# Performance work log

Measured on AMD Instinct MI355X. Metric: run time of the kernel, lower is better.

Reference implementation:

```python
import jax, jax.numpy as jnp
import numpy as np

B, T, I, H = 64, 512, 1024, 1024

def setup_inputs() -> dict:
    key = jax.random.key(0)
    k1, k2, k3, k4, k5 = jax.random.split(key, 5)
    s_x = 1.0 / np.sqrt(I)
    s_h = 1.0 / np.sqrt(H)
    return {
        "x": jax.random.normal(k1, (B, T, I), dtype=jnp.float32),
        "Wx": jax.random.uniform(k2, (I, H), minval=-s_x, maxval=s_x, dtype=jnp.float32),
        "bx": jax.random.uniform(k3, (H,), minval=-s_x, maxval=s_x, dtype=jnp.float32),
        "Wh": jax.random.uniform(k4, (H, H), minval=-s_h, maxval=s_h, dtype=jnp.float32),
        "bh": jax.random.uniform(k5, (H,), minval=-s_h, maxval=s_h, dtype=jnp.float32),
    }

def reference(x, Wx, bx, Wh, bh):
    # Precompute input projections for all timesteps in one big GEMM: [B,T,H]
    xproj = jnp.einsum("bti,ih->bth", x, Wx) + bx + bh
    h0 = jnp.zeros((x.shape[0], Wh.shape[0]), dtype=x.dtype)

    def step(h, xp_t):
        h_new = jnp.tanh(xp_t + h @ Wh)
        return h_new, h_new

    # scan over time: xproj transposed to [T,B,H]
    h_last, outs = jax.lax.scan(step, h0, jnp.swapaxes(xproj, 0, 1))
    return jnp.swapaxes(outs, 0, 1), h_last
```

## Files before the change

### kernel.cpp

```cpp
#include <hip/hip_runtime.h>


#define Bdim 64
#define Tdim 512
#define Idim 1024
#define Hdim 1024
#define Mdim (Bdim * Tdim)

typedef __attribute__((ext_vector_type(8))) short bf16x8;
typedef __attribute__((ext_vector_type(4))) float f32x4;
typedef __attribute__((ext_vector_type(4))) unsigned int u32x4;

__device__ __forceinline__ float tanh_fast(float x) {
  float e = __expf(2.0f * x);
  return 1.0f - 2.0f / (e + 1.0f);
}
__device__ __forceinline__ unsigned int f2bf(float f) {
  unsigned int u = __float_as_uint(f);
  return (u + 0x7FFFu + ((u >> 16) & 1u)) >> 16;
}
__device__ __forceinline__ unsigned int pack2(float lo, float hi) {
  return f2bf(lo) | (f2bf(hi) << 16);
}

__global__ __launch_bounds__(256) void cvt_transpose(
    const float* __restrict__ src, unsigned short* __restrict__ dst) {
  __shared__ float t[32][33];
  const int bx = blockIdx.x * 32;
  const int by = blockIdx.y * 32;
  const int ty = threadIdx.x >> 3;
  const int tx = threadIdx.x & 7;
  float4 v = *(const float4*)&src[(size_t)(by + ty) * 1024 + bx + tx * 4];
  t[ty][tx * 4 + 0] = v.x; t[ty][tx * 4 + 1] = v.y;
  t[ty][tx * 4 + 2] = v.z; t[ty][tx * 4 + 3] = v.w;
  __syncthreads();
  ushort4 o;
  o.x = (unsigned short)f2bf(t[tx * 4 + 0][ty]);
  o.y = (unsigned short)f2bf(t[tx * 4 + 1][ty]);
  o.z = (unsigned short)f2bf(t[tx * 4 + 2][ty]);
  o.w = (unsigned short)f2bf(t[tx * 4 + 3][ty]);
  *(ushort4*)&dst[(size_t)(bx + ty) * 1024 + by + tx * 4] = o;
}

__global__ __launch_bounds__(256) void xg_mfma(
    const float* __restrict__ X,
    const unsigned short* __restrict__ WxT,
    const float* __restrict__ bx, const float* __restrict__ bh,
    float* __restrict__ C) {
  __shared__ char sAB[16384] __attribute__((aligned(16)));
  char* sA = sAB;
  char* sB = sAB + 8192;
  const int tid = threadIdx.x;
  const int m0 = blockIdx.y * 128;
  const int n0 = blockIdx.x * 128;
  const int w = tid >> 6, l = tid & 63;
  const int wm = (w >> 1) * 64, wn = (w & 1) * 64;
  const int r2 = tid >> 1, kh = tid & 1;

  f32x4 acc[4][4];
#pragma unroll
  for (int i = 0; i < 4; ++i)
#pragma unroll
    for (int j = 0; j < 4; ++j) acc[i][j] = (f32x4){0.f, 0.f, 0.f, 0.f};

  for (int k0 = 0; k0 < Idim; k0 += 32) {
    const float* xa = &X[(size_t)(m0 + r2) * Idim + k0 + kh * 16];
    float4 a0 = *(const float4*)(xa + 0), a1 = *(const float4*)(xa + 4);
    float4 a2 = *(const float4*)(xa + 8), a3 = *(const float4*)(xa + 12);
    const char* wb = (const char*)&WxT[(size_t)(n0 + r2) * Idim + k0 + kh * 16];
    u32x4 b0 = *(const u32x4*)wb;
    u32x4 b1 = *(const u32x4*)(wb + 16);
    __syncthreads();
    u32x4 pa0 = {pack2(a0.x, a0.y), pack2(a0.z, a0.w),
                 pack2(a1.x, a1.y), pack2(a1.z, a1.w)};
    u32x4 pa1 = {pack2(a2.x, a2.y), pack2(a2.z, a2.w),
                 pack2(a3.x, a3.y), pack2(a3.z, a3.w)};
    const int sw = (r2 & 7) << 4;
    const int rb = r2 * 64 + kh * 32;
    *(u32x4*)(sA + ((rb + 0) ^ sw)) = pa0;
    *(u32x4*)(sA + ((rb + 16) ^ sw)) = pa1;
    *(u32x4*)(sB + ((rb + 0) ^ sw)) = b0;
    *(u32x4*)(sB + ((rb + 16) ^ sw)) = b1;
    __syncthreads();
    bf16x8 af[4], bf[4];
#pragma unroll
    for (int i = 0; i < 4; ++i) {
      int ra = wm + i * 16 + (l & 15);
      af[i] = *(const bf16x8*)(sA + ((ra * 64 + (l >> 4) * 16) ^ ((ra & 7) << 4)));
      int rn = wn + i * 16 + (l & 15);
      bf[i] = *(const bf16x8*)(sB + ((rn * 64 + (l >> 4) * 16) ^ ((rn & 7) << 4)));
    }
#pragma unroll
    for (int i = 0; i < 4; ++i)
#pragma unroll
      for (int j = 0; j < 4; ++j)
        acc[i][j] = __builtin_amdgcn_mfma_f32_16x16x32_bf16(af[i], bf[j],
                                                            acc[i][j], 0, 0, 0);
  }
  float bias[4];
#pragma unroll
  for (int j = 0; j < 4; ++j) {
    int cc = n0 + wn + j * 16 + (l & 15);
    bias[j] = bx[cc] + bh[cc];
  }
#pragma unroll
  for (int i = 0; i < 4; ++i) {
    int rbase = m0 + wm + i * 16 + (l >> 4) * 4;
#pragma unroll
    for (int j = 0; j < 4; ++j) {
      int cc = n0 + wn + j * 16 + (l & 15);
#pragma unroll
      for (int r = 0; r < 4; ++r)
        C[(size_t)(rbase + r) * Hdim + cc] = acc[i][j][r] + bias[j];
    }
  }
}

__global__ void clear_flags(unsigned int* flags) {
  __hip_atomic_store(&flags[threadIdx.x], 0u, __ATOMIC_RELAXED,
                     __HIP_MEMORY_SCOPE_AGENT);
}

__global__ __launch_bounds__(512, 2) void rnn_scan(
    const unsigned short* __restrict__ WhT,
    float* __restrict__ out,
    float* __restrict__ hlast,
    unsigned int* hbuf,
    unsigned int* flags) {
  const int bid = blockIdx.x;
  const int c = bid & 7;
  const int m = bid >> 3;
  const int tid = threadIdx.x;
  const int w = tid >> 6;
  const int l = tid & 63;
  const int n0 = m * 128;

  __shared__ char smem[16384 + 33792] __attribute__((aligned(16)));
  char* const smh = smem;
  char* const smp = smem + 16384;

  bf16x8 bfrag[32];
  {
    const int kb = (w << 7) + ((l >> 4) << 3);
    const int col = n0 + (l & 15);
#pragma unroll
    for (int nt = 0; nt < 8; ++nt)
#pragma unroll
      for (int kt = 0; kt < 4; ++kt)
        bfrag[nt * 4 + kt] =
            *(const bf16x8*)&WhT[(size_t)(col + nt * 16) * 1024 + kb + kt * 32];
  }
#pragma unroll
  for (int i = 0; i < 32; ++i) asm volatile("" : "+v"(bfrag[i]));

  const int c0 = l * 2;
  const int b_abs = c * 8 + w;
  const int nt0 = c0 >> 4;
  const int lane0 = ((w >> 2) << 4) | (c0 & 15);
  const int regb = (w & 3) * 4;
  const size_t orow = (size_t)b_abs * ((size_t)Tdim * Hdim) + n0 + c0;
  unsigned int* const myflag = &flags[c * 32 + m];
  const unsigned int* const pollf = &flags[c * 32 + (l & 7)];

  float2 xp = *(const float2*)&out[orow];

  for (int t = 0; t < Tdim; ++t) {
    float sum0 = 0.f, sum1 = 0.f;
    if (t > 0) {
      const int arow = l & 7;
      const int ab = arow * 2048 + (w << 8) + ((l >> 4) << 4);
      const int sw2 = arow << 4;
      bf16x8 af0 = *(const bf16x8*)(smh + ((ab + 0) ^ sw2));
      bf16x8 af1 = *(const bf16x8*)(smh + ((ab + 64) ^ sw2));
      bf16x8 af2 = *(const bf16x8*)(smh + ((ab + 128) ^ sw2));
      bf16x8 af3 = *(const bf16x8*)(smh + ((ab + 192) ^ sw2));
#pragma unroll
      for (int nt = 0; nt < 8; ++nt) {
        f32x4 a = {0.f, 0.f, 0.f, 0.f};
        a = __builtin_amdgcn_mfma_f32_16x16x32_bf16(af0, bfrag[nt * 4 + 0], a, 0, 0, 0);
        a = __builtin_amdgcn_mfma_f32_16x16x32_bf16(af1, bfrag[nt * 4 + 1], a, 0, 0, 0);
        a = __builtin_amdgcn_mfma_f32_16x16x32_bf16(af2, bfrag[nt * 4 + 2], a, 0, 0, 0);
        a = __builtin_amdgcn_mfma_f32_16x16x32_bf16(af3, bfrag[nt * 4 + 3], a, 0, 0, 0);
        if (l < 32)
          *(f32x4*)(smp + (((w * 8 + nt) * 33 + l) << 4)) = a;
      }
      asm volatile("s_waitcnt lgkmcnt(0)" ::: "memory");
      __builtin_amdgcn_s_barrier();
      asm volatile("" ::: "memory");
#pragma unroll
      for (int w8 = 0; w8 < 8; ++w8) {
        const char* p = smp + (((w8 * 8 + nt0) * 33 + lane0) << 4) + regb;
        sum0 += *(const float*)p;
        sum1 += *(const float*)(p + 16);
      }
    }
    float h0 = tanh_fast(xp.x + sum0);
    float h1 = tanh_fast(xp.y + sum1);
    if (t == Tdim - 1) {
      *(float2*)&out[orow + (size_t)t * Hdim] = make_float2(h0, h1);
      *(float2*)&hlast[(size_t)b_abs * Hdim + n0 + c0] = make_float2(h0, h1);
      break;
    }
    const int par = (t + 1) & 1;
    const unsigned int tp1 = (unsigned int)(t + 1);
    {
      unsigned int* pubp = hbuf + (size_t)par * 32768 + (size_t)b_abs * 512 +
                           m * 64 + l;
      unsigned int pv = pack2(h0, h1);
      asm volatile("global_store_dword %0, %1, off sc0 sc1"
                   :: "v"(pubp), "v"(pv) : "memory");
    }
    if (w != 7) {
      *(float2*)&out[orow + (size_t)t * Hdim] = make_float2(h0, h1);
      xp = *(const float2*)&out[orow + (size_t)(t + 1) * Hdim];
      asm volatile("s_waitcnt vmcnt(2)" ::: "memory");
    } else {
      asm volatile("s_waitcnt vmcnt(0)" ::: "memory");
    }
    __builtin_amdgcn_s_barrier();
    asm volatile("" ::: "memory");
    if (tid == 0)
      __hip_atomic_store(myflag, tp1, __ATOMIC_RELAXED,
                         __HIP_MEMORY_SCOPE_AGENT);
    if (w == 7) {
      for (;;) {
        unsigned int v;
        asm volatile(
            "global_load_dword %0, %1, off sc0 sc1\n\ts_waitcnt vmcnt(0)"
            : "=v"(v) : "v"(pollf) : "memory");
        if (__ballot(v >= tp1) == ~0ull) break;
        __builtin_amdgcn_s_sleep(1);
      }
    }
    __builtin_amdgcn_s_barrier();
    asm volatile("" ::: "memory");
    {
      const char* srcp = (const char*)hbuf + (size_t)par * 131072 +
                         (size_t)b_abs * 2048 + l * 32;
      u32x4 d0, d1;
      asm volatile(
          "global_load_dwordx4 %0, %2, off sc0 sc1\n\t"
          "global_load_dwordx4 %1, %2, off offset:16 sc0 sc1\n\t"
          "s_waitcnt vmcnt(0)"
          : "=&v"(d0), "=&v"(d1) : "v"(srcp) : "memory");
      __builtin_amdgcn_sched_barrier(0);
      const int base = w * 2048 + l * 32;
      const int swz = w << 4;
      *(u32x4*)(smh + (base ^ swz)) = d0;
      *(u32x4*)(smh + ((base + 16) ^ swz)) = d1;
    }
    if (w == 7) {
      *(float2*)&out[orow + (size_t)t * Hdim] = make_float2(h0, h1);
      xp = *(const float2*)&out[orow + (size_t)(t + 1) * Hdim];
    }
    asm volatile("s_waitcnt lgkmcnt(0)" ::: "memory");
    __builtin_amdgcn_s_barrier();
    asm volatile("" ::: "memory");
  }
}

extern "C" void kernel_launch(void* const* d_in, const int* in_sizes, int n_in,
                              void* d_out, int out_size, void* d_ws,
                              size_t ws_size, hipStream_t stream) {
  const float* x  = (const float*)d_in[0];
  const float* Wx = (const float*)d_in[1];
  const float* bx = (const float*)d_in[2];
  const float* Wh = (const float*)d_in[3];
  const float* bh = (const float*)d_in[4];
  float* out = (float*)d_out;
  float* hlast = out + (size_t)Bdim * Tdim * Hdim;
  unsigned int* flags = (unsigned int*)d_ws;
  unsigned int* hbuf = (unsigned int*)((char*)d_ws + 4096);
  unsigned short* WxT = (unsigned short*)((char*)d_ws + 4096 + 262144);
  unsigned short* WhT = (unsigned short*)((char*)d_ws + 4096 + 262144 + 2097152);

  clear_flags<<<1, dim3(256), 0, stream>>>(flags);
  dim3 gt(32, 32);
  cvt_transpose<<<gt, dim3(256), 0, stream>>>(Wx, WxT);
  cvt_transpose<<<gt, dim3(256), 0, stream>>>(Wh, WhT);
  xg_mfma<<<dim3(Hdim / 128, Mdim / 128), dim3(256), 0, stream>>>(x, WxT, bx,
                                                                  bh, out);
  rnn_scan<<<dim3(64), dim3(512), 0, stream>>>(WhT, out, hlast, hbuf, flags);
}
```

Measured before the change: 1.561 ms.

## Load recurrent A fragments directly from global, drop LDS staging and barrier

Each wave now loads its bf16 MFMA A-fragments of the previous hidden state straight from the global exchange buffer into registers. Previously each wave cooperatively copied an 8-row slab into swizzled shared memory, then read fragments back after an extra barrier. This removes the shared-memory staging, one barrier and the LDS pressure per timestep. In exchange it issues four scattered global loads per lane on the critical path instead of two contiguous ones, and the out store and xproj prefetch now sit after the poll rather than overlapping the flag wait.

```diff
diff --git a/kernel.cpp b/kernel.cpp
--- a/kernel.cpp
+++ b/kernel.cpp
@@ -135,9 +135,7 @@
   const int l = tid & 63;
   const int n0 = m * 128;
 
-  __shared__ char smem[16384 + 33792] __attribute__((aligned(16)));
-  char* const smh = smem;
-  char* const smp = smem + 16384;
+  __shared__ char smp[33792] __attribute__((aligned(16)));
 
   bf16x8 bfrag[32];
   {
@@ -161,19 +159,15 @@
   const size_t orow = (size_t)b_abs * ((size_t)Tdim * Hdim) + n0 + c0;
   unsigned int* const myflag = &flags[c * 32 + m];
   const unsigned int* const pollf = &flags[c * 32 + (l & 7)];
+  const char* const afbase = (const char*)hbuf +
+      (size_t)(c * 8 + (l & 7)) * 2048 + (size_t)((w << 8) + ((l >> 4) << 4));
 
   float2 xp = *(const float2*)&out[orow];
+  bf16x8 af0 = {}, af1 = {}, af2 = {}, af3 = {};
 
   for (int t = 0; t < Tdim; ++t) {
     float sum0 = 0.f, sum1 = 0.f;
     if (t > 0) {
-      const int arow = l & 7;
-      const int ab = arow * 2048 + (w << 8) + ((l >> 4) << 4);
-      const int sw2 = arow << 4;
-      bf16x8 af0 = *(const bf16x8*)(smh + ((ab + 0) ^ sw2));
-      bf16x8 af1 = *(const bf16x8*)(smh + ((ab + 64) ^ sw2));
-      bf16x8 af2 = *(const bf16x8*)(smh + ((ab + 128) ^ sw2));
-      bf16x8 af3 = *(const bf16x8*)(smh + ((ab + 192) ^ sw2));
 #pragma unroll
       for (int nt = 0; nt < 8; ++nt) {
         f32x4 a = {0.f, 0.f, 0.f, 0.f};
@@ -207,15 +201,9 @@
       unsigned int* pubp = hbuf + (size_t)par * 32768 + (size_t)b_abs * 512 +
                            m * 64 + l;
       unsigned int pv = pack2(h0, h1);
-      asm volatile("global_store_dword %0, %1, off sc0 sc1"
-                   :: "v"(pubp), "v"(pv) : "memory");
-    }
-    if (w != 7) {
-      *(float2*)&out[orow + (size_t)t * Hdim] = make_float2(h0, h1);
-      xp = *(const float2*)&out[orow + (size_t)(t + 1) * Hdim];
-      asm volatile("s_waitcnt vmcnt(2)" ::: "memory");
-    } else {
-      asm volatile("s_waitcnt vmcnt(0)" ::: "memory");
+      asm volatile(
+          "global_store_dword %0, %1, off sc0 sc1\n\ts_waitcnt vmcnt(0)"
+          :: "v"(pubp), "v"(pv) : "memory");
     }
     __builtin_amdgcn_s_barrier();
     asm volatile("" ::: "memory");
@@ -235,27 +223,19 @@
     __builtin_amdgcn_s_barrier();
     asm volatile("" ::: "memory");
     {
-      const char* srcp = (const char*)hbuf + (size_t)par * 131072 +
-                         (size_t)b_abs * 2048 + l * 32;
-      u32x4 d0, d1;
+      const char* srcp = afbase + (size_t)par * 131072;
       asm volatile(
-          "global_load_dwordx4 %0, %2, off sc0 sc1\n\t"
-          "global_load_dwordx4 %1, %2, off offset:16 sc0 sc1\n\t"
+          "global_load_dwordx4 %0, %4, off sc0 sc1\n\t"
+          "global_load_dwordx4 %1, %4, off offset:64 sc0 sc1\n\t"
+          "global_load_dwordx4 %2, %4, off offset:128 sc0 sc1\n\t"
+          "global_load_dwordx4 %3, %4, off offset:192 sc0 sc1\n\t"
           "s_waitcnt vmcnt(0)"
-          : "=&v"(d0), "=&v"(d1) : "v"(srcp) : "memory");
+          : "=&v"(af0), "=&v"(af1), "=&v"(af2), "=&v"(af3)
+          : "v"(srcp) : "memory");
       __builtin_amdgcn_sched_barrier(0);
-      const int base = w * 2048 + l * 32;
-      const int swz = w << 4;
-      *(u32x4*)(smh + (base ^ swz)) = d0;
-      *(u32x4*)(smh + ((base + 16) ^ swz)) = d1;
-    }
-    if (w == 7) {
-      *(float2*)&out[orow + (size_t)t * Hdim] = make_float2(h0, h1);
-      xp = *(const float2*)&out[orow + (size_t)(t + 1) * Hdim];
-    }
-    asm volatile("s_waitcnt lgkmcnt(0)" ::: "memory");
-    __builtin_amdgcn_s_barrier();
-    asm volatile("" ::: "memory");
+    }
+    *(float2*)&out[orow + (size_t)t * Hdim] = make_float2(h0, h1);
+    xp = *(const float2*)&out[orow + (size_t)(t + 1) * Hdim];
   }
 }
 
```

Result: slower. 1.867 ms (+19.6%).

## Fuse input-projection GEMM into recurrent scan kernel with per-time-chunk gating

Applied to the files above, without the earlier changes.

Merges the input-projection GEMM and the recurrent scan into one launch. 64 blocks run the scan while the remaining blocks compute GEMM tiles with 128x256 tiles. Each GEMM tile bumps a counter for its 128-timestep chunk, and the scan waits on that counter before entering each chunk. This is meant to hide most of the GEMM time behind the serial, latency-bound scan. The risks are that GEMM blocks compete with the scan blocks for CU time and memory bandwidth, and that the design depends on co-residency for forward progress. It also simplifies the per-step store and wait ordering and slightly lengthens the poll sleep.

```diff
diff --git a/kernel.cpp b/kernel.cpp
--- a/kernel.cpp
+++ b/kernel.cpp
@@ -42,100 +42,106 @@
   *(ushort4*)&dst[(size_t)(bx + ty) * 1024 + by + tx * 4] = o;
 }
 
-__global__ __launch_bounds__(256) void xg_mfma(
-    const float* __restrict__ X,
-    const unsigned short* __restrict__ WxT,
-    const float* __restrict__ bx, const float* __restrict__ bh,
-    float* __restrict__ C) {
-  __shared__ char sAB[16384] __attribute__((aligned(16)));
-  char* sA = sAB;
-  char* sB = sAB + 8192;
-  const int tid = threadIdx.x;
-  const int m0 = blockIdx.y * 128;
-  const int n0 = blockIdx.x * 128;
-  const int w = tid >> 6, l = tid & 63;
-  const int wm = (w >> 1) * 64, wn = (w & 1) * 64;
-  const int r2 = tid >> 1, kh = tid & 1;
-
-  f32x4 acc[4][4];
-#pragma unroll
-  for (int i = 0; i < 4; ++i)
-#pragma unroll
-    for (int j = 0; j < 4; ++j) acc[i][j] = (f32x4){0.f, 0.f, 0.f, 0.f};
-
-  for (int k0 = 0; k0 < Idim; k0 += 32) {
-    const float* xa = &X[(size_t)(m0 + r2) * Idim + k0 + kh * 16];
-    float4 a0 = *(const float4*)(xa + 0), a1 = *(const float4*)(xa + 4);
-    float4 a2 = *(const float4*)(xa + 8), a3 = *(const float4*)(xa + 12);
-    const char* wb = (const char*)&WxT[(size_t)(n0 + r2) * Idim + k0 + kh * 16];
-    u32x4 b0 = *(const u32x4*)wb;
-    u32x4 b1 = *(const u32x4*)(wb + 16);
-    __syncthreads();
-    u32x4 pa0 = {pack2(a0.x, a0.y), pack2(a0.z, a0.w),
-                 pack2(a1.x, a1.y), pack2(a1.z, a1.w)};
-    u32x4 pa1 = {pack2(a2.x, a2.y), pack2(a2.z, a2.w),
-                 pack2(a3.x, a3.y), pack2(a3.z, a3.w)};
-    const int sw = (r2 & 7) << 4;
-    const int rb = r2 * 64 + kh * 32;
-    *(u32x4*)(sA + ((rb + 0) ^ sw)) = pa0;
-    *(u32x4*)(sA + ((rb + 16) ^ sw)) = pa1;
-    *(u32x4*)(sB + ((rb + 0) ^ sw)) = b0;
-    *(u32x4*)(sB + ((rb + 16) ^ sw)) = b1;
-    __syncthreads();
-    bf16x8 af[4], bf[4];
-#pragma unroll
-    for (int i = 0; i < 4; ++i) {
-      int ra = wm + i * 16 + (l & 15);
-      af[i] = *(const bf16x8*)(sA + ((ra * 64 + (l >> 4) * 16) ^ ((ra & 7) << 4)));
-      int rn = wn + i * 16 + (l & 15);
-      bf[i] = *(const bf16x8*)(sB + ((rn * 64 + (l >> 4) * 16) ^ ((rn & 7) << 4)));
-    }
-#pragma unroll
-    for (int i = 0; i < 4; ++i)
-#pragma unroll
-      for (int j = 0; j < 4; ++j)
-        acc[i][j] = __builtin_amdgcn_mfma_f32_16x16x32_bf16(af[i], bf[j],
-                                                            acc[i][j], 0, 0, 0);
-  }
-  float bias[4];
-#pragma unroll
-  for (int j = 0; j < 4; ++j) {
-    int cc = n0 + wn + j * 16 + (l & 15);
-    bias[j] = bx[cc] + bh[cc];
-  }
-#pragma unroll
-  for (int i = 0; i < 4; ++i) {
-    int rbase = m0 + wm + i * 16 + (l >> 4) * 4;
-#pragma unroll
-    for (int j = 0; j < 4; ++j) {
-      int cc = n0 + wn + j * 16 + (l & 15);
-#pragma unroll
-      for (int r = 0; r < 4; ++r)
-        C[(size_t)(rbase + r) * Hdim + cc] = acc[i][j][r] + bias[j];
-    }
-  }
-}
-
 __global__ void clear_flags(unsigned int* flags) {
   __hip_atomic_store(&flags[threadIdx.x], 0u, __ATOMIC_RELAXED,
                      __HIP_MEMORY_SCOPE_AGENT);
 }
 
-__global__ __launch_bounds__(512, 2) void rnn_scan(
+__global__ __launch_bounds__(512, 2) void fused(
+    const float* __restrict__ X,
+    const unsigned short* __restrict__ WxT,
     const unsigned short* __restrict__ WhT,
+    const float* __restrict__ bx, const float* __restrict__ bh,
     float* __restrict__ out,
     float* __restrict__ hlast,
-    unsigned int* hbuf,
-    unsigned int* flags) {
+    unsigned int* hbuf, unsigned int* flags) {
+  __shared__ char smem[50176] __attribute__((aligned(16)));
+  unsigned int* counters = flags + 256;
   const int bid = blockIdx.x;
-  const int c = bid & 7;
-  const int m = bid >> 3;
   const int tid = threadIdx.x;
   const int w = tid >> 6;
   const int l = tid & 63;
+
+  if (bid >= 64) {
+    const int gid = bid - 64;
+    const int mt = gid >> 2;
+    const int np = gid & 3;
+    const int m0 = mt * 128, n0 = np * 256;
+    const int tc = mt & 3;
+    char* const sA = smem;
+    char* const sB = smem + 8192;
+    const int half = w >> 2, w2 = w & 3;
+    const int wm = (w2 >> 1) * 64, wn = half * 128 + (w2 & 1) * 64;
+    const int rA = tid >> 2, kA = tid & 3;
+    const int rB = tid >> 1, kB = tid & 1;
+
+    f32x4 acc[4][4];
+#pragma unroll
+    for (int i = 0; i < 4; ++i)
+#pragma unroll
+      for (int j = 0; j < 4; ++j) acc[i][j] = (f32x4){0.f, 0.f, 0.f, 0.f};
+
+    for (int k0 = 0; k0 < Idim; k0 += 32) {
+      const float* xa = &X[(size_t)(m0 + rA) * Idim + k0 + kA * 8];
+      float4 a0 = *(const float4*)xa, a1 = *(const float4*)(xa + 4);
+      const char* wb =
+          (const char*)&WxT[(size_t)(n0 + rB) * Idim + k0 + kB * 16];
+      u32x4 b0 = *(const u32x4*)wb, b1 = *(const u32x4*)(wb + 16);
+      __syncthreads();
+      u32x4 pa = {pack2(a0.x, a0.y), pack2(a0.z, a0.w),
+                  pack2(a1.x, a1.y), pack2(a1.z, a1.w)};
+      *(u32x4*)(sA + ((rA * 64 + kA * 16) ^ ((rA & 7) << 4))) = pa;
+      const int rbB = rB * 64 + kB * 32, swB = (rB & 7) << 4;
+      *(u32x4*)(sB + (rbB ^ swB)) = b0;
+      *(u32x4*)(sB + ((rbB + 16) ^ swB)) = b1;
+      __syncthreads();
+      bf16x8 af[4], bf[4];
+#pragma unroll
+      for (int i = 0; i < 4; ++i) {
+        int ra = wm + i * 16 + (l & 15);
+        af[i] = *(const bf16x8*)(sA + ((ra * 64 + (l >> 4) * 16) ^ ((ra & 7) << 4)));
+        int rn = wn + i * 16 + (l & 15);
+        bf[i] = *(const bf16x8*)(sB + ((rn * 64 + (l >> 4) * 16) ^ ((rn & 7) << 4)));
+      }
+#pragma unroll
+      for (int i = 0; i < 4; ++i)
+#pragma unroll
+        for (int j = 0; j < 4; ++j)
+          acc[i][j] = __builtin_amdgcn_mfma_f32_16x16x32_bf16(af[i], bf[j],
+                                                              acc[i][j], 0, 0, 0);
+    }
+    float bias[4];
+#pragma unroll
+    for (int j = 0; j < 4; ++j) {
+      int cc = n0 + wn + j * 16 + (l & 15);
+      bias[j] = bx[cc] + bh[cc];
+    }
+#pragma unroll
+    for (int i = 0; i < 4; ++i) {
+      int rbase = m0 + wm + i * 16 + (l >> 4) * 4;
+#pragma unroll
+      for (int j = 0; j < 4; ++j) {
+        int cc = n0 + wn + j * 16 + (l & 15);
+#pragma unroll
+        for (int r = 0; r < 4; ++r) {
+          float v = acc[i][j][r] + bias[j];
+          float* p = &out[(size_t)(rbase + r) * Hdim + cc];
+          asm volatile("global_store_dword %0, %1, off sc0 sc1"
+                       :: "v"(p), "v"(v) : "memory");
+        }
+      }
+    }
+    asm volatile("s_waitcnt vmcnt(0)" ::: "memory");
+    __syncthreads();
+    if (tid == 0)
+      __hip_atomic_fetch_add(&counters[tc], 1u, __ATOMIC_RELAXED,
+                             __HIP_MEMORY_SCOPE_AGENT);
+    return;
+  }
+
+  const int c = bid & 7;
+  const int m = bid >> 3;
   const int n0 = m * 128;
-
-  __shared__ char smem[16384 + 33792] __attribute__((aligned(16)));
   char* const smh = smem;
   char* const smp = smem + 16384;
 
@@ -150,8 +156,6 @@
         bfrag[nt * 4 + kt] =
             *(const bf16x8*)&WhT[(size_t)(col + nt * 16) * 1024 + kb + kt * 32];
   }
-#pragma unroll
-  for (int i = 0; i < 32; ++i) asm volatile("" : "+v"(bfrag[i]));
 
   const int c0 = l * 2;
   const int b_abs = c * 8 + w;
@@ -162,6 +166,22 @@
   unsigned int* const myflag = &flags[c * 32 + m];
   const unsigned int* const pollf = &flags[c * 32 + (l & 7)];
 
+  auto gate = [&](int tc2) {
+    if (tid == 0) {
+      const unsigned int* cp = &counters[tc2];
+      for (;;) {
+        unsigned int v;
+        asm volatile(
+            "global_load_dword %0, %1, off sc0 sc1\n\ts_waitcnt vmcnt(0)"
+            : "=v"(v) : "v"(cp) : "memory");
+        if (v >= 256u) break;
+        __builtin_amdgcn_s_sleep(16);
+      }
+    }
+    __syncthreads();
+  };
+
+  gate(0);
   float2 xp = *(const float2*)&out[orow];
 
   for (int t = 0; t < Tdim; ++t) {
@@ -201,22 +221,17 @@
       *(float2*)&hlast[(size_t)b_abs * Hdim + n0 + c0] = make_float2(h0, h1);
       break;
     }
+    if (((t + 1) & 127) == 0) gate((t + 1) >> 7);
     const int par = (t + 1) & 1;
     const unsigned int tp1 = (unsigned int)(t + 1);
-    {
-      unsigned int* pubp = hbuf + (size_t)par * 32768 + (size_t)b_abs * 512 +
-                           m * 64 + l;
-      unsigned int pv = pack2(h0, h1);
-      asm volatile("global_store_dword %0, %1, off sc0 sc1"
-                   :: "v"(pubp), "v"(pv) : "memory");
-    }
-    if (w != 7) {
-      *(float2*)&out[orow + (size_t)t * Hdim] = make_float2(h0, h1);
-      xp = *(const float2*)&out[orow + (size_t)(t + 1) * Hdim];
-      asm volatile("s_waitcnt vmcnt(2)" ::: "memory");
-    } else {
-      asm volatile("s_waitcnt vmcnt(0)" ::: "memory");
-    }
+    __hip_atomic_store(&hbuf[(size_t)par * 32768 + (size_t)b_abs * 512 +
+                             m * 64 + l],
+                       pack2(h0, h1), __ATOMIC_RELAXED,
+                       __HIP_MEMORY_SCOPE_AGENT);
+    asm volatile("" ::: "memory");
+    *(float2*)&out[orow + (size_t)t * Hdim] = make_float2(h0, h1);
+    xp = *(const float2*)&out[orow + (size_t)(t + 1) * Hdim];
+    asm volatile("s_waitcnt vmcnt(2)" ::: "memory");
     __builtin_amdgcn_s_barrier();
     asm volatile("" ::: "memory");
     if (tid == 0)
@@ -229,9 +244,10 @@
             "global_load_dword %0, %1, off sc0 sc1\n\ts_waitcnt vmcnt(0)"
             : "=v"(v) : "v"(pollf) : "memory");
         if (__ballot(v >= tp1) == ~0ull) break;
-        __builtin_amdgcn_s_sleep(1);
-      }
-    }
+        __builtin_amdgcn_s_sleep(2);
+      }
+    }
+    asm volatile("" ::: "memory");
     __builtin_amdgcn_s_barrier();
     asm volatile("" ::: "memory");
     {
@@ -249,10 +265,6 @@
       *(u32x4*)(smh + (base ^ swz)) = d0;
       *(u32x4*)(smh + ((base + 16) ^ swz)) = d1;
     }
-    if (w == 7) {
-      *(float2*)&out[orow + (size_t)t * Hdim] = make_float2(h0, h1);
-      xp = *(const float2*)&out[orow + (size_t)(t + 1) * Hdim];
-    }
     asm volatile("s_waitcnt lgkmcnt(0)" ::: "memory");
     __builtin_amdgcn_s_barrier();
     asm volatile("" ::: "memory");
@@ -274,11 +286,10 @@
   unsigned short* WxT = (unsigned short*)((char*)d_ws + 4096 + 262144);
   unsigned short* WhT = (unsigned short*)((char*)d_ws + 4096 + 262144 + 2097152);
 
-  clear_flags<<<1, dim3(256), 0, stream>>>(flags);
+  clear_flags<<<1, dim3(512), 0, stream>>>(flags);
   dim3 gt(32, 32);
   cvt_transpose<<<gt, dim3(256), 0, stream>>>(Wx, WxT);
   cvt_transpose<<<gt, dim3(256), 0, stream>>>(Wh, WhT);
-  xg_mfma<<<dim3(Hdim / 128, Mdim / 128), dim3(256), 0, stream>>>(x, WxT, bx,
-                                                                  bh, out);
-  rnn_scan<<<dim3(64), dim3(512), 0, stream>>>(WhT, out, hlast, hbuf, flags);
-}
+  fused<<<dim3(64 + 1024), dim3(512), 0, stream>>>(x, WxT, WhT, bx, bh, out,
+                                                   hlast, hbuf, flags);
+}
```

After: 1.605 ms. +2.8%, slower.
